# Kernel tuning notes

Measured on AMD Instinct MI355X. Metric: run time of the kernel, lower is better.

Reference implementation:

```python
import jax, jax.numpy as jnp
import numpy as np

GRID = 7
NUM_CLASSES = 80
LAMBDA_COORD = 5.0
LAMBDA_NOOBJ = 0.5
EPS_IOU = 1e-06
EPS_SQRT = 1e-06


def setup_inputs() -> dict:
    key = jax.random.key(0)
    k1, k2, k3 = jax.random.split(key, 3)
    B = 4096
    D = 10 + NUM_CLASSES
    pred = jax.random.uniform(k1, (B, GRID, GRID, D), dtype=jnp.float32)
    target = jax.random.uniform(k2, (B, GRID, GRID, D), dtype=jnp.float32)
    # confidence channel of target must be exactly 1.0 for object cells
    obj = (jax.random.uniform(k3, (B, GRID, GRID)) < 0.25).astype(jnp.float32)
    target = target.at[..., 4].set(obj)
    return {"pred": pred, "target": target}


def _iou(b1, b2):
    # b1, b2: [..., 4] boxes as (cx, cy, w, h) in image coords
    x1, y1, w1, h1 = b1[..., 0], b1[..., 1], b1[..., 2], b1[..., 3]
    x2, y2, w2, h2 = b2[..., 0], b2[..., 1], b2[..., 2], b2[..., 3]
    ix_min = jnp.maximum(x1 - w1 / 2, x2 - w2 / 2)
    iy_min = jnp.maximum(y1 - h1 / 2, y2 - h2 / 2)
    ix_max = jnp.minimum(x1 + w1 / 2, x2 + w2 / 2)
    iy_max = jnp.minimum(y1 + h1 / 2, y2 + h2 / 2)
    iw = jnp.clip(ix_max - ix_min, 0.0)
    ih = jnp.clip(iy_max - iy_min, 0.0)
    inter = iw * ih
    union = w1 * h1 + w2 * h2 - inter
    return inter / (union + EPS_IOU)


def _forward(pred, target):
    S = pred.shape[1]
    gy = jnp.arange(S, dtype=pred.dtype).reshape(1, S, 1)
    gx = jnp.arange(S, dtype=pred.dtype).reshape(1, 1, S)

    def to_img(box5):  # [B,S,S,5] cell-relative -> [B,S,S,4] image coords
        cx = (gx + box5[..., 0]) / S
        cy = (gy + box5[..., 1]) / S
        return jnp.stack([cx, cy, box5[..., 2], box5[..., 3]], axis=-1)

    box1 = pred[..., 0:5]
    box2 = pred[..., 5:10]
    tbox = target[..., 0:5]

    iou1 = _iou(to_img(box1), to_img(tbox))
    iou2 = _iou(to_img(box2), to_img(tbox))
    resp1 = iou1 > iou2  # box1 responsible if strictly greater (matches `if iou1 > iou2`)
    best = jnp.where(resp1[..., None], box1, box2)  # [B,S,S,5]

    obj = target[..., 4] == 1.0  # [B,S,S]
    objf = obj.astype(pred.dtype)
    n_obj = jnp.sum(objf)
    n_cells = jnp.asarray(pred.shape[0] * S * S, pred.dtype)

    # coord: mean-of-2 xy MSE + mean-of-2 sqrt(wh) MSE per responsible box
    dxy2 = jnp.sum((best[..., 0:2] - tbox[..., 0:2]) ** 2, axis=-1)
    swh_p = jnp.sqrt(jnp.clip(best[..., 2:4], EPS_SQRT))
    swh_t = jnp.sqrt(jnp.clip(tbox[..., 2:4], EPS_SQRT))
    dwh2 = jnp.sum((swh_p - swh_t) ** 2, axis=-1)
    coord_per = 0.5 * dxy2 + 0.5 * dwh2
    coord_loss = jnp.sum(coord_per * objf) / jnp.maximum(n_obj, 1.0)

    # confidence: obj cells -> (best_conf - 1)^2 (count 1); noobj -> lam*(c1^2 + c2^2) (count 2)
    conf_obj = (best[..., 4] - 1.0) ** 2
    conf_noobj = LAMBDA_NOOBJ * (pred[..., 4] ** 2 + pred[..., 9] ** 2)
    conf_sum = jnp.sum(jnp.where(obj, conf_obj, conf_noobj))
    conf_count = n_obj + 2.0 * (n_cells - n_obj)
    conf_loss = conf_sum / jnp.maximum(conf_count, 1.0)

    # class: mean over classes per obj cell
    class_per = jnp.mean((pred[..., 10:] - target[..., 10:]) ** 2, axis=-1)
    class_loss = jnp.sum(class_per * objf) / jnp.maximum(n_obj, 1.0)

    return LAMBDA_COORD * coord_loss + conf_loss + class_loss


def reference(pred, target):
    return _forward(pred, target)
```

## Files before the change

kernel.cpp:

```cpp
#include <hip/hip_runtime.h>

#define GRID_S 7
#define NUM_CLASSES 80
#define D_DIM 90
#define LAMBDA_COORD 5.0f
#define LAMBDA_NOOBJ 0.5f
#define EPS_IOU 1e-6f
#define EPS_SQRT 1e-6f

#define TILE 64
#define TILE_F (TILE * D_DIM)
#define TILE_F4 (TILE_F / 4)

__device__ __forceinline__ void async_ld16(const float4* g, float4* l) {
    __builtin_amdgcn_global_load_lds(
        (const __attribute__((address_space(1))) void*)g,
        (__attribute__((address_space(3))) void*)l,
        16, 0, 0);
}

__device__ __forceinline__ float iou_img(float cx1, float cy1, float w1, float h1,
                                         float cx2, float cy2, float w2, float h2) {
    float ixmin = fmaxf(cx1 - w1 * 0.5f, cx2 - w2 * 0.5f);
    float iymin = fmaxf(cy1 - h1 * 0.5f, cy2 - h2 * 0.5f);
    float ixmax = fminf(cx1 + w1 * 0.5f, cx2 + w2 * 0.5f);
    float iymax = fminf(cy1 + h1 * 0.5f, cy2 + h2 * 0.5f);
    float iw = fmaxf(ixmax - ixmin, 0.0f);
    float ih = fmaxf(iymax - iymin, 0.0f);
    float inter = iw * ih;
    float uni = w1 * h1 + w2 * h2 - inter;
    return inter / (uni + EPS_IOU);
}

__global__ __launch_bounds__(256) void yolo_cell_kernel(
        const float* __restrict__ pred, const float* __restrict__ targ,
        float* __restrict__ part, int ncells) {
    __shared__ float sp[TILE_F];
    __shared__ float st[TILE_F];

    const int tid = threadIdx.x;
    const int base_cell = blockIdx.x * TILE;
    const int valid = min(TILE, ncells - base_cell);
    const int nf = valid * D_DIM;
    const int nf4 = nf >> 2;

    const size_t base_f = (size_t)base_cell * D_DIM;
    const float4* p4 = (const float4*)(pred + base_f);
    const float4* t4 = (const float4*)(targ + base_f);
    float4* sp4 = (float4*)sp;
    float4* st4 = (float4*)st;
    for (int i = tid; i < nf4; i += 256) async_ld16(p4 + i, sp4 + i);
    for (int i = tid; i < nf4; i += 256) async_ld16(t4 + i, st4 + i);
    for (int i = (nf4 << 2) + tid; i < nf; i += 256) {
        sp[i] = pred[base_f + i];
        st[i] = targ[base_f + i];
    }
    __syncthreads();

    const int cell = tid & 63;
    const int g = tid >> 6;
    float v_obj = 0.0f, v_coord = 0.0f, v_conf = 0.0f, v_cls = 0.0f;

    if (cell < valid) {
        const float* cp = sp + cell * D_DIM;
        const float* ct = st + cell * D_DIM;
        const float2* cp2 = (const float2*)cp;
        const float2* ct2 = (const float2*)ct;

        float objf = (ct[4] == 1.0f) ? 1.0f : 0.0f;

        float cls = 0.0f;
        const int s2 = 5 + 10 * g;
        #pragma unroll
        for (int j = 0; j < 10; ++j) {
            float2 p = cp2[s2 + j];
            float2 t = ct2[s2 + j];
            float dx = p.x - t.x;
            float dy = p.y - t.y;
            cls = fmaf(dx, dx, cls);
            cls = fmaf(dy, dy, cls);
        }
        v_cls = cls * (1.0f / (float)NUM_CLASSES) * objf;

        if (g == 0) {
            const int gcell = base_cell + cell;
            const int gxy = gcell % (GRID_S * GRID_S);
            const float gy = (float)(gxy / GRID_S);
            const float gx = (float)(gxy % GRID_S);

            float b1x = cp[0], b1y = cp[1], b1w = cp[2], b1h = cp[3], b1c = cp[4];
            float b2x = cp[5], b2y = cp[6], b2w = cp[7], b2h = cp[8], b2c = cp[9];
            float tbx = ct[0], tby = ct[1], tbw = ct[2], tbh = ct[3];

            const float invS = 1.0f / (float)GRID_S;
            float c1x = (gx + b1x) * invS, c1y = (gy + b1y) * invS;
            float c2x = (gx + b2x) * invS, c2y = (gy + b2y) * invS;
            float ctx = (gx + tbx) * invS, cty = (gy + tby) * invS;

            float iou1 = iou_img(c1x, c1y, b1w, b1h, ctx, cty, tbw, tbh);
            float iou2 = iou_img(c2x, c2y, b2w, b2h, ctx, cty, tbw, tbh);
            bool resp1 = iou1 > iou2;

            float bx = resp1 ? b1x : b2x;
            float by = resp1 ? b1y : b2y;
            float bw = resp1 ? b1w : b2w;
            float bh = resp1 ? b1h : b2h;
            float bc = resp1 ? b1c : b2c;

            bool obj = (objf == 1.0f);

            float ddx = bx - tbx, ddy = by - tby;
            float dxy2 = ddx * ddx + ddy * ddy;
            float swpw = sqrtf(fmaxf(bw, EPS_SQRT));
            float swph = sqrtf(fmaxf(bh, EPS_SQRT));
            float swtw = sqrtf(fmaxf(tbw, EPS_SQRT));
            float swth = sqrtf(fmaxf(tbh, EPS_SQRT));
            float dw = swpw - swtw, dh = swph - swth;
            float dwh2 = dw * dw + dh * dh;
            float coord = 0.5f * dxy2 + 0.5f * dwh2;

            float dco = bc - 1.0f;
            float conf_obj = dco * dco;
            float conf_noobj = LAMBDA_NOOBJ * (b1c * b1c + b2c * b2c);

            v_obj = objf;
            v_coord = coord * objf;
            v_conf = obj ? conf_obj : conf_noobj;
        }
    }

    #pragma unroll
    for (int off = 32; off > 0; off >>= 1) {
        v_obj   += __shfl_down(v_obj, off, 64);
        v_coord += __shfl_down(v_coord, off, 64);
        v_conf  += __shfl_down(v_conf, off, 64);
        v_cls   += __shfl_down(v_cls, off, 64);
    }

    __shared__ float red[4][4];
    const int lane = tid & 63;
    const int wid = tid >> 6;
    if (lane == 0) {
        red[wid][0] = v_obj;
        red[wid][1] = v_coord;
        red[wid][2] = v_conf;
        red[wid][3] = v_cls;
    }
    __syncthreads();
    if (tid < 4) {
        float s = red[0][tid] + red[1][tid] + red[2][tid] + red[3][tid];
        part[(size_t)blockIdx.x * 4 + tid] = s;
    }
}

__global__ __launch_bounds__(1024) void yolo_final_kernel(
        const float* __restrict__ part, float* __restrict__ out,
        int nblocks, int ncells) {
    const int tid = threadIdx.x;
    float a0 = 0.0f, a1 = 0.0f, a2 = 0.0f, a3 = 0.0f;
    const float4* p4 = (const float4*)part;
    for (int b = tid; b < nblocks; b += 1024) {
        float4 v = p4[b];
        a0 += v.x; a1 += v.y; a2 += v.z; a3 += v.w;
    }
    #pragma unroll
    for (int off = 32; off > 0; off >>= 1) {
        a0 += __shfl_down(a0, off, 64);
        a1 += __shfl_down(a1, off, 64);
        a2 += __shfl_down(a2, off, 64);
        a3 += __shfl_down(a3, off, 64);
    }
    __shared__ float red[16][4];
    const int wid = tid >> 6;
    if ((tid & 63) == 0) {
        red[wid][0] = a0; red[wid][1] = a1; red[wid][2] = a2; red[wid][3] = a3;
    }
    __syncthreads();
    if (tid == 0) {
        float n_obj = 0.0f, coord = 0.0f, conf = 0.0f, cls = 0.0f;
        #pragma unroll
        for (int w = 0; w < 16; ++w) {
            n_obj += red[w][0]; coord += red[w][1];
            conf  += red[w][2]; cls   += red[w][3];
        }
        float n_cells = (float)ncells;
        float conf_count = n_obj + 2.0f * (n_cells - n_obj);
        float denom = fmaxf(n_obj, 1.0f);
        out[0] = LAMBDA_COORD * coord / denom + conf / fmaxf(conf_count, 1.0f) + cls / denom;
    }
}

extern "C" void kernel_launch(void* const* d_in, const int* in_sizes, int n_in,
                              void* d_out, int out_size, void* d_ws, size_t ws_size,
                              hipStream_t stream) {
    const float* pred = (const float*)d_in[0];
    const float* targ = (const float*)d_in[1];
    float* part = (float*)d_ws;
    float* out = (float*)d_out;

    const int ncells = in_sizes[0] / D_DIM;
    const int ntiles = (ncells + TILE - 1) / TILE;

    yolo_cell_kernel<<<ntiles, 256, 0, stream>>>(pred, targ, part, ncells);
    yolo_final_kernel<<<1, 1024, 0, stream>>>(part, out, ntiles, ncells);
}
```

Measured before the change: 158.4 us.

## Split loss into streaming class-MSE blocks and per-cell box blocks

Drops the LDS tile staging. A fixed pool of 630 blocks now streams both tensors as flat float4s with a grid-stride loop and weights each element's squared difference by a per-lane class mask and the owning cell's objectness flag. Separate blocks compute the box, IoU and confidence terms with one thread per cell, reading only the first ten fields. This aims for fully coalesced wide loads across the whole GPU, at the cost of extra scattered objectness reads from the target tensor, a hardcoded grid size and stride assumptions (the 45-lane pattern needs GA*256 divisible by 45), and roughly twice the bytes touched for the first ten fields.

Result: slower. 163.2 us (+3.1%).

```diff
diff --git a/kernel.cpp b/kernel.cpp
--- a/kernel.cpp
+++ b/kernel.cpp
@@ -8,16 +8,7 @@
 #define EPS_IOU 1e-6f
 #define EPS_SQRT 1e-6f
 
-#define TILE 64
-#define TILE_F (TILE * D_DIM)
-#define TILE_F4 (TILE_F / 4)
-
-__device__ __forceinline__ void async_ld16(const float4* g, float4* l) {
-    __builtin_amdgcn_global_load_lds(
-        (const __attribute__((address_space(1))) void*)g,
-        (__attribute__((address_space(3))) void*)l,
-        16, 0, 0);
-}
+#define GA 630
 
 __device__ __forceinline__ float iou_img(float cx1, float cy1, float w1, float h1,
                                          float cx2, float cy2, float w2, float h2) {
@@ -32,66 +23,68 @@
     return inter / (uni + EPS_IOU);
 }
 
-__global__ __launch_bounds__(256) void yolo_cell_kernel(
+__global__ __launch_bounds__(256) void yolo_main_kernel(
         const float* __restrict__ pred, const float* __restrict__ targ,
         float* __restrict__ part, int ncells) {
-    __shared__ float sp[TILE_F];
-    __shared__ float st[TILE_F];
-
     const int tid = threadIdx.x;
-    const int base_cell = blockIdx.x * TILE;
-    const int valid = min(TILE, ncells - base_cell);
-    const int nf = valid * D_DIM;
-    const int nf4 = nf >> 2;
-
-    const size_t base_f = (size_t)base_cell * D_DIM;
-    const float4* p4 = (const float4*)(pred + base_f);
-    const float4* t4 = (const float4*)(targ + base_f);
-    float4* sp4 = (float4*)sp;
-    float4* st4 = (float4*)st;
-    for (int i = tid; i < nf4; i += 256) async_ld16(p4 + i, sp4 + i);
-    for (int i = tid; i < nf4; i += 256) async_ld16(t4 + i, st4 + i);
-    for (int i = (nf4 << 2) + tid; i < nf; i += 256) {
-        sp[i] = pred[base_f + i];
-        st[i] = targ[base_f + i];
-    }
-    __syncthreads();
-
-    const int cell = tid & 63;
-    const int g = tid >> 6;
     float v_obj = 0.0f, v_coord = 0.0f, v_conf = 0.0f, v_cls = 0.0f;
 
-    if (cell < valid) {
-        const float* cp = sp + cell * D_DIM;
-        const float* ct = st + cell * D_DIM;
-        const float2* cp2 = (const float2*)cp;
-        const float2* ct2 = (const float2*)ct;
-
-        float objf = (ct[4] == 1.0f) ? 1.0f : 0.0f;
-
-        float cls = 0.0f;
-        const int s2 = 5 + 10 * g;
+    if (blockIdx.x < GA) {
+        const int NF4 = (ncells * D_DIM) >> 2;
+        const int T = GA * 256;
+        const int t = blockIdx.x * 256 + tid;
+        const int phase = t % 45;
+        int g = t / 45;
+        const int GSTRIDE = T / 45;
+
+        float w0[4], w1[4];
         #pragma unroll
-        for (int j = 0; j < 10; ++j) {
-            float2 p = cp2[s2 + j];
-            float2 t = ct2[s2 + j];
-            float dx = p.x - t.x;
-            float dy = p.y - t.y;
-            cls = fmaf(dx, dx, cls);
-            cls = fmaf(dy, dy, cls);
-        }
-        v_cls = cls * (1.0f / (float)NUM_CLASSES) * objf;
-
-        if (g == 0) {
-            const int gcell = base_cell + cell;
-            const int gxy = gcell % (GRID_S * GRID_S);
+        for (int e = 0; e < 4; ++e) {
+            int fe = phase * 4 + e;
+            int ce = (fe >= 90) ? 1 : 0;
+            int de = fe - 90 * ce;
+            float cw = (de >= 10) ? 1.0f : 0.0f;
+            w0[e] = ce ? 0.0f : cw;
+            w1[e] = ce ? cw : 0.0f;
+        }
+
+        const float4* p4 = (const float4*)pred;
+        const float4* t4 = (const float4*)targ;
+        float acc = 0.0f;
+        for (int j = t; j < NF4; j += T, g += GSTRIDE) {
+            float4 p = p4[j];
+            float4 tv = t4[j];
+            const float* ob = targ + (size_t)g * 180;
+            float o0 = ob[4];
+            float o1 = ob[94];
+            float f0 = (o0 == 1.0f) ? 1.0f : 0.0f;
+            float f1 = (o1 == 1.0f) ? 1.0f : 0.0f;
+            float d0 = p.x - tv.x;
+            float d1 = p.y - tv.y;
+            float d2 = p.z - tv.z;
+            float d3 = p.w - tv.w;
+            acc = fmaf(d0 * d0, fmaf(w1[0], f1, w0[0] * f0), acc);
+            acc = fmaf(d1 * d1, fmaf(w1[1], f1, w0[1] * f0), acc);
+            acc = fmaf(d2 * d2, fmaf(w1[2], f1, w0[2] * f0), acc);
+            acc = fmaf(d3 * d3, fmaf(w1[3], f1, w0[3] * f0), acc);
+        }
+        v_cls = acc * (1.0f / (float)NUM_CLASSES);
+    } else {
+        const int cell = (blockIdx.x - GA) * 256 + tid;
+        if (cell < ncells) {
+            const float2* cp2 = (const float2*)(pred + (size_t)cell * D_DIM);
+            const float2* ct2 = (const float2*)(targ + (size_t)cell * D_DIM);
+            float2 pA = cp2[0], pB = cp2[1], pC = cp2[2], pD = cp2[3], pE = cp2[4];
+            float2 tA = ct2[0], tB = ct2[1], tC = ct2[2];
+
+            float b1x = pA.x, b1y = pA.y, b1w = pB.x, b1h = pB.y, b1c = pC.x;
+            float b2x = pC.y, b2y = pD.x, b2w = pD.y, b2h = pE.x, b2c = pE.y;
+            float tbx = tA.x, tby = tA.y, tbw = tB.x, tbh = tB.y;
+            float tobj = tC.x;
+
+            const int gxy = cell % (GRID_S * GRID_S);
             const float gy = (float)(gxy / GRID_S);
             const float gx = (float)(gxy % GRID_S);
-
-            float b1x = cp[0], b1y = cp[1], b1w = cp[2], b1h = cp[3], b1c = cp[4];
-            float b2x = cp[5], b2y = cp[6], b2w = cp[7], b2h = cp[8], b2c = cp[9];
-            float tbx = ct[0], tby = ct[1], tbw = ct[2], tbh = ct[3];
-
             const float invS = 1.0f / (float)GRID_S;
             float c1x = (gx + b1x) * invS, c1y = (gy + b1y) * invS;
             float c2x = (gx + b2x) * invS, c2y = (gy + b2y) * invS;
@@ -107,7 +100,8 @@
             float bh = resp1 ? b1h : b2h;
             float bc = resp1 ? b1c : b2c;
 
-            bool obj = (objf == 1.0f);
+            bool obj = (tobj == 1.0f);
+            float objf = obj ? 1.0f : 0.0f;
 
             float ddx = bx - tbx, ddy = by - tby;
             float dxy2 = ddx * ddx + ddy * ddy;
@@ -136,7 +130,6 @@
         v_conf  += __shfl_down(v_conf, off, 64);
         v_cls   += __shfl_down(v_cls, off, 64);
     }
-
     __shared__ float red[4][4];
     const int lane = tid & 63;
     const int wid = tid >> 6;
@@ -199,8 +192,9 @@
     float* out = (float*)d_out;
 
     const int ncells = in_sizes[0] / D_DIM;
-    const int ntiles = (ncells + TILE - 1) / TILE;
-
-    yolo_cell_kernel<<<ntiles, 256, 0, stream>>>(pred, targ, part, ncells);
-    yolo_final_kernel<<<1, 1024, 0, stream>>>(part, out, ntiles, ncells);
-}
+    const int GB = (ncells + 255) / 256;
+    const int nblocks = GA + GB;
+
+    yolo_main_kernel<<<nblocks, 256, 0, stream>>>(pred, targ, part, ncells);
+    yolo_final_kernel<<<1, 1024, 0, stream>>>(part, out, nblocks, ncells);
+}
```
